# Performance work log

Hardware: AMD Instinct MI355X
Metric: run time of the kernel (lower is better)

Reference implementation:

```python
import jax, jax.numpy as jnp
import numpy as np

B, N, H, E, P = 2, 20000, 128, 200000, 3


def _mlp2(x, w1, b1, w2, b2):
    # Linear -> SiLU -> Linear
    return jax.nn.silu(x @ w1 + b1) @ w2 + b2


def setup_inputs() -> dict:
    key = jax.random.key(0)
    ks = iter(jax.random.split(key, 40))
    def nrm(shape, s=0.05):
        return jax.random.normal(next(ks), shape, dtype=jnp.float32) * s
    inp = {
        "features": jax.random.normal(next(ks), (B, N, H), dtype=jnp.float32),
        "positions": jax.random.normal(next(ks), (B, N, P), dtype=jnp.float32),
        "edge_index_up": jax.random.randint(next(ks), (2, E), 0, N, dtype=jnp.int32),
        "edge_index_down": jax.random.randint(next(ks), (2, E), 0, N, dtype=jnp.int32),
        "degree_up": jax.random.uniform(next(ks), (N,), minval=1.0, maxval=32.0, dtype=jnp.float32),
        "degree_down": jax.random.uniform(next(ks), (N,), minval=1.0, maxval=32.0, dtype=jnp.float32),
    }
    for name in ("up", "down"):
        inp[f"w_msg1_{name}"] = nrm((2 * H + 1, H)); inp[f"b_msg1_{name}"] = jnp.zeros((H,), jnp.float32)
        inp[f"w_msg2_{name}"] = nrm((H, H));         inp[f"b_msg2_{name}"] = jnp.zeros((H,), jnp.float32)
        inp[f"w_pos1_{name}"] = nrm((H, H));         inp[f"b_pos1_{name}"] = jnp.zeros((H,), jnp.float32)
        inp[f"w_pos2_{name}"] = nrm((H, 1));         inp[f"b_pos2_{name}"] = jnp.zeros((1,), jnp.float32)
    inp["w_upd1"] = nrm((2 * H, H)); inp["b_upd1"] = jnp.zeros((H,), jnp.float32)
    inp["w_upd2"] = nrm((H, H));     inp["b_upd2"] = jnp.zeros((H,), jnp.float32)
    return inp


def reference(features, positions, edge_index_up, edge_index_down, degree_up, degree_down,
              w_msg1_up, b_msg1_up, w_msg2_up, b_msg2_up,
              w_pos1_up, b_pos1_up, w_pos2_up, b_pos2_up,
              w_msg1_down, b_msg1_down, w_msg2_down, b_msg2_down,
              w_pos1_down, b_pos1_down, w_pos2_down, b_pos2_down,
              w_upd1, b_upd1, w_upd2, b_upd2):
    n_neighborhoods = 2
    msg_acc = jnp.zeros_like(features)
    pos_upd = jnp.zeros_like(positions)
    neighborhoods = [
        (edge_index_up, degree_up,
         (w_msg1_up, b_msg1_up, w_msg2_up, b_msg2_up),
         (w_pos1_up, b_pos1_up, w_pos2_up, b_pos2_up)),
        (edge_index_down, degree_down,
         (w_msg1_down, b_msg1_down, w_msg2_down, b_msg2_down),
         (w_pos1_down, b_pos1_down, w_pos2_down, b_pos2_down)),
    ]
    for edge_index, degree, msg_p, pos_p in neighborhoods:
        src, dst = edge_index[0], edge_index[1]
        h_src = features[:, src, :]                     # [B, E, H] gather
        h_dst = features[:, dst, :]                     # [B, E, H] gather
        rel_pos = positions[:, src, :] - positions[:, dst, :]  # [B, E, P]
        dist = jnp.linalg.norm(rel_pos, axis=-1, keepdims=True)  # [B, E, 1]
        msg_input = jnp.concatenate([h_src, h_dst, dist], axis=-1)  # [B, E, 2H+1]
        messages = _mlp2(msg_input, *msg_p)             # [B, E, H]
        agg = jnp.zeros_like(features).at[:, dst, :].add(messages)  # scatter-add over dim 1
        agg = agg / jnp.clip(degree, 1.0, None)[None, :, None]
        msg_acc = msg_acc + agg
        weights = jnp.tanh(_mlp2(messages, *pos_p))     # [B, E, 1]
        pos_upd = pos_upd + jnp.zeros_like(positions).at[:, dst, :].add(weights * rel_pos)
    feat_update = _mlp2(jnp.concatenate([features, msg_acc], axis=-1), w_upd1, b_upd1, w_upd2, b_upd2)
    updated_features = features + feat_update
    updated_positions = positions + pos_upd / n_neighborhoods
    return updated_features, updated_positions
```

## Files before the change

### kernel.cpp

```cpp
#include <hip/hip_runtime.h>

#define BB 2
#define NN 20000
#define HH 128
#define EE 200000
#define TR 64
#define NEB 3125
#define NBLK 79
#define NWG (2 * BB * NEB)

typedef unsigned short u16;
typedef __attribute__((ext_vector_type(4))) float f32x4;
typedef __bf16 bf16x8 __attribute__((ext_vector_type(8)));

#define MFMA(a, b, c) __builtin_amdgcn_mfma_f32_16x16x32_bf16((a), (b), (c), 0, 0, 0)

__device__ __forceinline__ float bf2f(u16 u) {
    union { unsigned int i; float f; } v; v.i = ((unsigned int)u) << 16; return v.f;
}
__device__ __forceinline__ u16 f2bf(float f) {
    union { __bf16 h; u16 u; } v; v.h = (__bf16)f; return v.u;
}
#if __has_builtin(__builtin_amdgcn_rcpf)
__device__ __forceinline__ float rcpf(float x) { return __builtin_amdgcn_rcpf(x); }
#else
__device__ __forceinline__ float rcpf(float x) { return 1.f / x; }
#endif
__device__ __forceinline__ float silu_f(float z) { return z * rcpf(1.f + __expf(-z)); }
__device__ __forceinline__ float ldv(const void* p, long i, int f) {
    return f ? ((const float*)p)[i] : bf2f(((const u16*)p)[i]);
}

__global__ __launch_bounds__(256) void detect_zero_kernel(const u16* __restrict__ f,
                                                          int* __restrict__ flag,
                                                          int* __restrict__ cnt) {
    int i = blockIdx.x * 256 + threadIdx.x;
    if (i < 40000) cnt[i] = 0;
    if (blockIdx.x == 0) {
        int tid = threadIdx.x;
        u16 v = f[tid * 2];
        int e = (v >> 7) & 0xFF;
        int ok = (e >= 101 && e <= 143) ? 1 : 0;
        __shared__ int c;
        if (tid == 0) c = 0;
        __syncthreads();
        atomicAdd(&c, ok);
        __syncthreads();
        if (tid == 0) *flag = (c < 200) ? 1 : 0;
    }
}

#define C5TOT 5281540
#define FTOT 180224
#define R0 5240000
#define R1 (R0 + C5TOT)
#define R2 (R1 + FTOT)
#define R3 (R2 + 2 * EE)
struct P18 { const void* p[18]; };
struct P8 { const void* w[8]; };

__global__ __launch_bounds__(256) void setup_kernel(
    P18 cp, P8 wf, const int* __restrict__ eu, const int* __restrict__ ed,
    float* __restrict__ ws_acc, u16* __restrict__ canon, u16* __restrict__ fbase,
    int* __restrict__ cnt_up, int* __restrict__ cnt_dn, const int* __restrict__ flag)
{
    long i = (long)blockIdx.x * 256 + threadIdx.x;
    if (i < R0) { ws_acc[i] = 0.f; return; }
    if (i < R1) {
        static const int off[19] = {
            0, 5120000, 5240000, 5260000, 5280000,
            5280128, 5280256, 5280384, 5280512, 5280640,
            5280642, 5280770, 5280898, 5281026, 5281154, 5281282,
            5281284, 5281412, 5281540 };
        static const int rsz[18] = {
            5120000, 120000, 20000, 20000,
            128, 128, 128, 128, 128, 1,
            128, 128, 128, 128, 128, 1,
            128, 128 };
        static const int soff[18] = {
            0, 0, 0, 0,
            32768, 0, 0, 0, 0, 0,
            32768, 0, 0, 0, 0, 0,
            0, 0 };
        int j = (int)(i - R0);
        int isf = *flag;
        int t = 0;
#pragma unroll 1
        while (j >= off[t + 1]) ++t;
        int k = j - off[t];
        u16 v = 0;
        if (k < rsz[t]) v = f2bf(ldv(cp.p[t], (long)soff[t] + k, isf));
        canon[j] = v;
        return;
    }
    if (i < R2) {
        static const int foff[9] = { 0, 32768, 49152, 65536, 98304, 114688,
                                     131072, 163840, 180224 };
        int j = (int)(i - R1);
        int isf = *flag;
        int t = 0;
#pragma unroll 1
        while (j >= foff[t + 1]) ++t;
        int m = j - foff[t];
        int jj = m & 7, lane = (m >> 3) & 63, nt = (m >> 9) & 7, kt = m >> 12;
        int k = kt * 32 + ((lane >> 4) * 8) + jj;
        int n = nt * 16 + (lane & 15);
        fbase[j] = f2bf(ldv(wf.w[t], (long)k * 128 + n, isf));
        return;
    }
    if (i < R3) {
        int e = (int)(i - R2);
        if (e < EE) atomicAdd(&cnt_up[eu[EE + e]], 1);
        else atomicAdd(&cnt_dn[ed[EE + e - EE]], 1);
    }
}

__global__ __launch_bounds__(256) void gemm_fuse_kernel(
    const void* __restrict__ w2u, const void* __restrict__ p1u,
    const void* __restrict__ b2u, const void* __restrict__ bp1u,
    const void* __restrict__ w2d, const void* __restrict__ p1d,
    const void* __restrict__ b2d, const void* __restrict__ bp1d,
    u16* __restrict__ fragu, u16* __restrict__ fragd,
    u16* __restrict__ cbp1u, u16* __restrict__ cbp1d,
    const int* __restrict__ flag)
{
    const int dir = blockIdx.x >> 6;
    const int idx = (blockIdx.x & 63) * 256 + threadIdx.x;
    const int k = idx >> 7, n = idx & 127;
    const int isf = *flag;
    const void* W2 = dir ? w2d : w2u;
    const void* P1 = dir ? p1d : p1u;
    float s = 0.f;
#pragma unroll 4
    for (int m = 0; m < 128; ++m)
        s += ldv(W2, (long)k * 128 + m, isf) * ldv(P1, (long)m * 128 + n, isf);
    u16* dst = dir ? fragd : fragu;
    dst[(((k >> 5) * 8 + (n >> 4)) * 64 + ((k >> 3) & 3) * 16 + (n & 15)) * 8 + (k & 7)] = f2bf(s);
    if (idx < 128) {
        const void* B2 = dir ? b2d : b2u;
        const void* BP1 = dir ? bp1d : bp1u;
        float t = 0.f;
#pragma unroll 4
        for (int m = 0; m < 128; ++m)
            t += ldv(B2, m, isf) * ldv(P1, (long)m * 128 + idx, isf);
        (dir ? cbp1d : cbp1u)[idx] = f2bf(t + ldv(BP1, idx, isf));
    }
}

struct SP { const int* cnt[2]; int* cur[2]; int* bsum[2]; };

__global__ __launch_bounds__(256) void scan1_kernel(SP p) {
    int half = blockIdx.x / NBLK;
    int b = blockIdx.x - half * NBLK;
    int t = threadIdx.x;
    int i = b * 256 + t;
    __shared__ int buf[256];
    int v = (i < NN) ? p.cnt[half][i] : 0;
    buf[t] = v;
    __syncthreads();
    for (int s = 1; s < 256; s <<= 1) {
        int x = (t >= s) ? buf[t - s] : 0;
        __syncthreads();
        buf[t] += x;
        __syncthreads();
    }
    if (i < NN) p.cur[half][i] = buf[t] - v;
    if (t == 255) p.bsum[half][b] = buf[255];
}

__global__ __launch_bounds__(256) void scan2_kernel(int* __restrict__ bu, int* __restrict__ bd) {
    __shared__ int buf[2][128];
    int half = threadIdx.x >> 7, t = threadIdx.x & 127;
    int* bs = half ? bd : bu;
    int v = (t < NBLK) ? bs[t] : 0;
    buf[half][t] = v;
    __syncthreads();
    for (int s = 1; s < 128; s <<= 1) {
        int x = (t >= s) ? buf[half][t - s] : 0;
        __syncthreads();
        buf[half][t] += x;
        __syncthreads();
    }
    if (t < NBLK) bs[t] = buf[half][t] - v;
}

__global__ void scatter2_kernel(const int* __restrict__ eu, const int* __restrict__ ed,
                                int* __restrict__ cu, const int* __restrict__ bu,
                                int* __restrict__ cd, const int* __restrict__ bd,
                                int* __restrict__ su, int* __restrict__ sd) {
    int e = blockIdx.x * 256 + threadIdx.x;
    if (e < EE) {
        int d = eu[EE + e];
        int p = atomicAdd(&cu[d], 1) + bu[d >> 8];
        su[p] = e;
    } else {
        e -= EE;
        if (e < EE) {
            int d = ed[EE + e];
            int p = atomicAdd(&cd[d], 1) + bd[d >> 8];
            sd[p] = e;
        }
    }
}

struct EP {
    const int* eidx; const int* es; const u16* deg;
    const u16* fW1; const u16* fW2; const u16* fP1;
    const u16* w1last; const u16* bias1; const u16* bias2;
    const u16* biasp1; const u16* wp2; const u16* biasp2;
};

__global__ __launch_bounds__(512, 6) void edge_kernel(
    const u16* __restrict__ feat, const u16* __restrict__ posit,
    EP up, EP dn,
    float* __restrict__ msg_base, float* __restrict__ pos_base)
{
    const int tid = threadIdx.x;
    const int lane = tid & 63;
    const int wv = tid >> 6;
    const int bid0 = blockIdx.x;
    const int xcd = bid0 & 7;
    const int bid = (xcd < 4 ? xcd * 1563 : 4 * 1563 + (xcd - 4) * 1562) + (bid0 >> 3);
    const int half = bid / (BB * NEB);
    const int rem = bid - half * (BB * NEB);
    const int bb = rem / NEB;
    const int s0 = (rem - bb * NEB) * TR;
    const EP P = half ? dn : up;
    float* msg_acc = msg_base + (size_t)bb * NN * HH;
    float* pos_acc = pos_base + (size_t)bb * NN * 3;

    __shared__ u16 sA[TR][136];
    __shared__ u16 sB[TR][136];
    __shared__ u16 sC[TR][136];
    __shared__ float sInv[TR];
    __shared__ float sWgt[TR];
    __shared__ int sDst[TR];

    const int wm = wv >> 2;
    const int wn = wv & 3;
    const int rbase = wm * 32;
    const int mrow = lane & 15;
    const int kq = (lane >> 4) * 8;
    const int crow = (lane >> 4) * 4;
    const int ccol = lane & 15;

    {
        const int r = tid >> 3, part = tid & 7;
        int slot = s0 + r; if (slot >= EE) slot = EE - 1;
        int e = P.es[slot];
        int s = P.eidx[e];
        int d = P.eidx[EE + e];
        if (part == 0) {
            sDst[r] = d;
            sInv[r] = 1.f / fmaxf(bf2f(P.deg[d]), 1.f);
            const u16* ps = posit + ((size_t)bb * NN + s) * 3;
            const u16* pd = posit + ((size_t)bb * NN + d) * 3;
            float dx = bf2f(ps[0]) - bf2f(pd[0]);
            float dy = bf2f(ps[1]) - bf2f(pd[1]);
            float dz = bf2f(ps[2]) - bf2f(pd[2]);
            *(float4*)&sC[r][128] =
                make_float4(sqrtf(dx * dx + dy * dy + dz * dz), dx, dy, dz);
        }
        const uint4* fs = (const uint4*)(feat + ((size_t)bb * NN + s) * HH);
        const uint4* fd = (const uint4*)(feat + ((size_t)bb * NN + d) * HH);
        uint4* as = (uint4*)&sA[r][part * 16];
        uint4* ad = (uint4*)&sB[r][part * 16];
#pragma unroll
        for (int i = 0; i < 2; ++i) { as[i] = fs[part * 2 + i]; ad[i] = fd[part * 2 + i]; }
    }
    __syncthreads();

    f32x4 acc[2][2];
#pragma unroll
    for (int mt = 0; mt < 2; ++mt) {
        acc[mt][0] = (f32x4){0.f, 0.f, 0.f, 0.f};
        acc[mt][1] = (f32x4){0.f, 0.f, 0.f, 0.f};
    }
#pragma unroll
    for (int kt = 0; kt < 8; ++kt) {
        const u16* Xb = (kt < 4) ? &sA[0][0] : &sB[0][0];
        const int kk = (kt & 3) * 32 + kq;
        bf16x8 bw0 = *(const bf16x8*)(P.fW1 + (size_t)(((kt * 8 + wn * 2) * 64 + lane) * 8));
        bf16x8 bw1 = *(const bf16x8*)(P.fW1 + (size_t)(((kt * 8 + wn * 2 + 1) * 64 + lane) * 8));
#pragma unroll
        for (int mt = 0; mt < 2; ++mt) {
            bf16x8 a = *(const bf16x8*)(Xb + (rbase + mt * 16 + mrow) * 136 + kk);
            acc[mt][0] = MFMA(a, bw0, acc[mt][0]);
            acc[mt][1] = MFMA(a, bw1, acc[mt][1]);
        }
    }

#pragma unroll
    for (int n2 = 0; n2 < 2; ++n2) {
        const int col = (wn * 2 + n2) * 16 + ccol;
        const float wl = bf2f(P.w1last[col]);
        const float bb1 = bf2f(P.bias1[col]);
#pragma unroll
        for (int mt = 0; mt < 2; ++mt) {
#pragma unroll
            for (int r = 0; r < 4; ++r) {
                const int row = rbase + mt * 16 + crow + r;
                const float dist = ((const float*)&sC[row][128])[0];
                float z = fmaf(dist, wl, acc[mt][n2][r]) + bb1;
                sC[row][col] = f2bf(silu_f(z));
            }
        }
    }
    __syncthreads();

    f32x4 facc[2][4];
#pragma unroll
    for (int mt = 0; mt < 2; ++mt)
#pragma unroll
        for (int j = 0; j < 4; ++j) facc[mt][j] = (f32x4){0.f, 0.f, 0.f, 0.f};
    const int nt0 = wn * 4;
#pragma unroll
    for (int kt = 0; kt < 4; ++kt) {
        const int kk = kt * 32 + kq;
        bf16x8 bw[4];
#pragma unroll
        for (int j = 0; j < 4; ++j) {
            const int nt = nt0 + j;
            const size_t off = (nt & 8)
                ? (size_t)(16384 + ((kt * 8 + (nt & 7)) * 64 + lane) * 8)
                : (size_t)(((kt * 8 + nt) * 64 + lane) * 8);
            bw[j] = *(const bf16x8*)(P.fW2 + off);
        }
#pragma unroll
        for (int mt = 0; mt < 2; ++mt) {
            bf16x8 a = *(const bf16x8*)(&sC[0][0] + (rbase + mt * 16 + mrow) * 136 + kk);
#pragma unroll
            for (int j = 0; j < 4; ++j) facc[mt][j] = MFMA(a, bw[j], facc[mt][j]);
        }
    }

    if (wn < 2) {
#pragma unroll
        for (int j = 0; j < 4; ++j) {
            const int col = (nt0 + j) * 16 + ccol;
            const float b2v = bf2f(P.bias2[col]);
#pragma unroll
            for (int mt = 0; mt < 2; ++mt) {
#pragma unroll
                for (int r = 0; r < 4; ++r) {
                    const int row = rbase + mt * 16 + crow + r;
                    sA[row][col] = f2bf(facc[mt][j][r] + b2v);
                }
            }
        }
    } else {
#pragma unroll
        for (int j = 0; j < 4; ++j) {
            const int col = (nt0 - 8 + j) * 16 + ccol;
            const float fbv = bf2f(P.biasp1[col]);
#pragma unroll
            for (int mt = 0; mt < 2; ++mt) {
#pragma unroll
                for (int r = 0; r < 4; ++r) {
                    const int row = rbase + mt * 16 + crow + r;
                    sB[row][col] = f2bf(silu_f(facc[mt][j][r] + fbv));
                }
            }
        }
    }
    __syncthreads();

    {
        const int scol = tid & 127;
        const int r0 = (tid >> 7) * 16;
        float vals[16];
#pragma unroll
        for (int j = 0; j < 16; ++j) vals[j] = bf2f(sA[r0 + j][scol]);
        float accv = 0.f;
        int dprev = sDst[r0];
        float invprev = sInv[r0];
#pragma unroll
        for (int j = 0; j < 16; ++j) {
            const int r = r0 + j;
            int dcur = sDst[r];
            if (dcur != dprev) {
                unsafeAtomicAdd(&msg_acc[(size_t)dprev * HH + scol], accv * invprev);
                accv = 0.f; dprev = dcur; invprev = sInv[r];
            }
            accv += (s0 + r < EE) ? vals[j] : 0.f;
        }
        unsafeAtomicAdd(&msg_acc[(size_t)dprev * HH + scol], accv * invprev);
    }

    {
        const int r = tid >> 2, q = tid & 3;
        if (r < TR) {
            const unsigned* t32 = (const unsigned*)&sB[r][q * 32];
            const unsigned* w32 = (const unsigned*)(P.wp2 + q * 32);
            float p = 0.f;
#pragma unroll
            for (int k = 0; k < 16; ++k) {
                unsigned a = t32[k], b = w32[k];
                union { unsigned i; float f; } al, ah, bl, bh;
                al.i = a << 16; ah.i = a & 0xffff0000u;
                bl.i = b << 16; bh.i = b & 0xffff0000u;
                p = fmaf(al.f, bl.f, p);
                p = fmaf(ah.f, bh.f, p);
            }
            p += __shfl_xor(p, 1);
            p += __shfl_xor(p, 2);
            if (q == 0)
                sWgt[r] = (s0 + r < EE) ? tanhf(p + bf2f(P.biasp2[0])) : 0.f;
        }
    }
    __syncthreads();

    if (tid < 12) {
        const int comp = tid % 3;
        const int r0 = (tid / 3) * 16;
        float accv = 0.f;
        int dprev = sDst[r0];
#pragma unroll
        for (int j = 0; j < 16; ++j) {
            const int r = r0 + j;
            int dcur = sDst[r];
            if (dcur != dprev) {
                if (accv != 0.f) unsafeAtomicAdd(&pos_acc[(size_t)dprev * 3 + comp], accv);
                accv = 0.f; dprev = dcur;
            }
            accv += sWgt[r] * ((const float*)&sC[r][128])[1 + comp];
        }
        if (accv != 0.f) unsafeAtomicAdd(&pos_acc[(size_t)dprev * 3 + comp], accv);
    }
}

__global__ __launch_bounds__(256) void update_kernel(
    const void* __restrict__ rawfeat, const void* __restrict__ rawpos,
    const u16* __restrict__ fU1, const u16* __restrict__ bu1,
    const u16* __restrict__ fU2, const u16* __restrict__ bu2,
    void* __restrict__ outp, const float* __restrict__ magg, const float* __restrict__ pacc,
    const int* __restrict__ flag)
{
    const int tid = threadIdx.x;
    const int lane = tid & 63;
    const int wv = tid >> 6;
    const int row0 = blockIdx.x * 64;
    const int isf = *flag;

    __shared__ u16 sA[64][136];
    __shared__ u16 sB[64][136];

    if (isf) {
        const float* fp = (const float*)rawfeat + (size_t)row0 * HH;
        for (int i = tid; i < 1024; i += 256) {
            int r = i >> 4, c = (i & 15) * 8;
            float4 v0 = *(const float4*)(fp + (size_t)r * HH + c);
            float4 v1 = *(const float4*)(fp + (size_t)r * HH + c + 4);
            uint4 o;
            o.x = (unsigned)f2bf(v0.x) | ((unsigned)f2bf(v0.y) << 16);
            o.y = (unsigned)f2bf(v0.z) | ((unsigned)f2bf(v0.w) << 16);
            o.z = (unsigned)f2bf(v1.x) | ((unsigned)f2bf(v1.y) << 16);
            o.w = (unsigned)f2bf(v1.z) | ((unsigned)f2bf(v1.w) << 16);
            *(uint4*)&sA[r][c] = o;
        }
    } else {
        const uint4* fp = (const uint4*)((const u16*)rawfeat + (size_t)row0 * HH);
        for (int i = tid; i < 1024; i += 256) {
            int r = i >> 4, c = i & 15;
            *(uint4*)&sA[r][c * 8] = fp[i];
        }
    }
    {
        const float4* am = (const float4*)(magg) + (size_t)row0 * 32;
        for (int i = tid; i < 2048; i += 256) {
            int r = i >> 5;
            float4 v = am[i];
            int c = (i & 31) * 4;
            sB[r][c + 0] = f2bf(v.x);
            sB[r][c + 1] = f2bf(v.y);
            sB[r][c + 2] = f2bf(v.z);
            sB[r][c + 3] = f2bf(v.w);
        }
    }
    __syncthreads();

    const int nt0 = wv * 2;
    const int mrow = lane & 15;
    const int kq = (lane >> 4) * 8;
    const int crow = (lane >> 4) * 4;
    const int ccol = lane & 15;

    f32x4 acc[4][2];
#pragma unroll
    for (int mt = 0; mt < 4; ++mt) {
        acc[mt][0] = (f32x4){0.f, 0.f, 0.f, 0.f};
        acc[mt][1] = (f32x4){0.f, 0.f, 0.f, 0.f};
    }
#pragma unroll
    for (int kt = 0; kt < 8; ++kt) {
        const u16* Xb = (kt < 4) ? &sA[0][0] : &sB[0][0];
        const int kk = (kt & 3) * 32 + kq;
        bf16x8 bw0 = *(const bf16x8*)(fU1 + (size_t)(((kt * 8 + nt0) * 64 + lane) * 8));
        bf16x8 bw1 = *(const bf16x8*)(fU1 + (size_t)(((kt * 8 + nt0 + 1) * 64 + lane) * 8));
#pragma unroll
        for (int mt = 0; mt < 4; ++mt) {
            bf16x8 a = *(const bf16x8*)(Xb + (mt * 16 + mrow) * 136 + kk);
            acc[mt][0] = MFMA(a, bw0, acc[mt][0]);
            acc[mt][1] = MFMA(a, bw1, acc[mt][1]);
        }
    }
    __syncthreads();

#pragma unroll
    for (int mt = 0; mt < 4; ++mt) {
#pragma unroll
        for (int n2 = 0; n2 < 2; ++n2) {
            const int col = (nt0 + n2) * 16 + ccol;
            const float bb = bf2f(bu1[col]);
#pragma unroll
            for (int r = 0; r < 4; ++r) {
                const int row = mt * 16 + crow + r;
                sB[row][col] = f2bf(silu_f(acc[mt][n2][r] + bb));
            }
        }
    }
    __syncthreads();

#pragma unroll
    for (int mt = 0; mt < 4; ++mt) {
        acc[mt][0] = (f32x4){0.f, 0.f, 0.f, 0.f};
        acc[mt][1] = (f32x4){0.f, 0.f, 0.f, 0.f};
    }
#pragma unroll
    for (int kt = 0; kt < 4; ++kt) {
        const int kk = kt * 32 + kq;
        bf16x8 bw0 = *(const bf16x8*)(fU2 + (size_t)(((kt * 8 + nt0) * 64 + lane) * 8));
        bf16x8 bw1 = *(const bf16x8*)(fU2 + (size_t)(((kt * 8 + nt0 + 1) * 64 + lane) * 8));
#pragma unroll
        for (int mt = 0; mt < 4; ++mt) {
            bf16x8 a = *(const bf16x8*)(&sB[0][0] + (mt * 16 + mrow) * 136 + kk);
            acc[mt][0] = MFMA(a, bw0, acc[mt][0]);
            acc[mt][1] = MFMA(a, bw1, acc[mt][1]);
        }
    }
#pragma unroll
    for (int mt = 0; mt < 4; ++mt) {
#pragma unroll
        for (int n2 = 0; n2 < 2; ++n2) {
            const int col = (nt0 + n2) * 16 + ccol;
            const float bb = bf2f(bu2[col]);
#pragma unroll
            for (int r = 0; r < 4; ++r) {
                const int row = mt * 16 + crow + r;
                const size_t idx = (size_t)(row0 + row) * HH + col;
                if (isf) {
                    float base = ((const float*)rawfeat)[idx];
                    ((float*)outp)[idx] = acc[mt][n2][r] + bb + base;
                } else {
                    float base = bf2f(sA[row][col]);
                    ((u16*)outp)[idx] = f2bf(acc[mt][n2][r] + bb + base);
                }
            }
        }
    }

    if (tid < 192) {
        int i = row0 * 3 + tid;
        float x = pacc[i];
        if (isf) {
            float base = ((const float*)rawpos)[i];
            ((float*)outp)[5120000 + i] = base + 0.5f * x;
        } else {
            float base = bf2f(((const u16*)rawpos)[i]);
            ((u16*)outp)[5120000 + i] = f2bf(base + 0.5f * x);
        }
    }
}

extern "C" void kernel_launch(void* const* d_in, const int* in_sizes, int n_in,
                              void* d_out, int out_size, void* d_ws, size_t ws_size,
                              hipStream_t stream)
{
    float* ws_msg  = (float*)d_ws;
    float* ws_pos  = (float*)((char*)d_ws + 20480000);
    int*   cnt_up  = (int*)((char*)d_ws + 20960000);
    int*   cnt_dn  = (int*)((char*)d_ws + 21040000);
    int*   cur_up  = (int*)((char*)d_ws + 21120000);
    int*   cur_dn  = (int*)((char*)d_ws + 21200000);
    int*   bsum_up = (int*)((char*)d_ws + 21280000);
    int*   bsum_dn = (int*)((char*)d_ws + 21280400);
    int*   es_up   = (int*)((char*)d_ws + 21280800);
    int*   es_dn   = (int*)((char*)d_ws + 22080800);
    u16*   fbase   = (u16*)((char*)d_ws + 22880800);
    u16*   canon   = (u16*)((char*)d_ws + 23241248);
    int*   flag    = (int*)((char*)d_ws + 33804328);
    if (ws_size < 33804332ULL) return;

    u16* f_m1u = fbase;
    u16* f_m2u = fbase + 32768;
    u16* f_p1u = fbase + 49152;
    u16* f_m1d = fbase + 65536;
    u16* f_m2d = fbase + 98304;
    u16* f_p1d = fbase + 114688;
    u16* f_u1  = fbase + 131072;
    u16* f_u2  = fbase + 163840;

    u16* cfeat  = canon;
    u16* cpos   = canon + 5120000;
    u16* cdgu   = canon + 5240000;
    u16* cdgd   = canon + 5260000;
    u16* cw1lu  = canon + 5280000;
    u16* cb1u   = canon + 5280128;
    u16* cb2u   = canon + 5280256;
    u16* cbp1u  = canon + 5280384;
    u16* cwp2u  = canon + 5280512;
    u16* cbp2u  = canon + 5280640;
    u16* cw1ld  = canon + 5280642;
    u16* cb1d   = canon + 5280770;
    u16* cb2d   = canon + 5280898;
    u16* cbp1d  = canon + 5281026;
    u16* cwp2d  = canon + 5281154;
    u16* cbp2d  = canon + 5281282;
    u16* cbu1   = canon + 5281284;
    u16* cbu2   = canon + 5281412;

    const int* ei_up = (const int*)d_in[2];
    const int* ei_dn = (const int*)d_in[3];

    detect_zero_kernel<<<157, 256, 0, stream>>>((const u16*)d_in[0], flag, cnt_up);

    P18 cp;
    cp.p[0] = d_in[0];  cp.p[1] = d_in[1];  cp.p[2] = d_in[4];  cp.p[3] = d_in[5];
    cp.p[4] = d_in[6];  cp.p[5] = d_in[7];  cp.p[6] = d_in[9];  cp.p[7] = d_in[11];
    cp.p[8] = d_in[12]; cp.p[9] = d_in[13];
    cp.p[10] = d_in[14]; cp.p[11] = d_in[15]; cp.p[12] = d_in[17]; cp.p[13] = d_in[19];
    cp.p[14] = d_in[20]; cp.p[15] = d_in[21];
    cp.p[16] = d_in[23]; cp.p[17] = d_in[25];
    P8 wsf;
    wsf.w[0] = d_in[6];  wsf.w[1] = d_in[8];  wsf.w[2] = d_in[10]; wsf.w[3] = d_in[14];
    wsf.w[4] = d_in[16]; wsf.w[5] = d_in[18]; wsf.w[6] = d_in[22]; wsf.w[7] = d_in[24];
    setup_kernel<<<(R3 + 255) / 256, 256, 0, stream>>>(cp, wsf, ei_up, ei_dn,
                                                       ws_msg, canon, fbase,
                                                       cnt_up, cnt_dn, flag);

    gemm_fuse_kernel<<<128, 256, 0, stream>>>(d_in[8], d_in[10], d_in[9], d_in[11],
                                              d_in[16], d_in[18], d_in[17], d_in[19],
                                              f_p1u, f_p1d, cbp1u, cbp1d, flag);

    SP sp;
    sp.cnt[0] = cnt_up; sp.cnt[1] = cnt_dn;
    sp.cur[0] = cur_up; sp.cur[1] = cur_dn;
    sp.bsum[0] = bsum_up; sp.bsum[1] = bsum_dn;
    scan1_kernel<<<2 * NBLK, 256, 0, stream>>>(sp);
    scan2_kernel<<<1, 256, 0, stream>>>(bsum_up, bsum_dn);
    scatter2_kernel<<<(2 * EE + 255) / 256, 256, 0, stream>>>(ei_up, ei_dn, cur_up, bsum_up,
                                                              cur_dn, bsum_dn, es_up, es_dn);

    EP up, dn;
    up.eidx = ei_up; up.es = es_up; up.deg = cdgu;
    up.fW1 = f_m1u; up.fW2 = f_m2u; up.fP1 = f_p1u;
    up.w1last = cw1lu; up.bias1 = cb1u; up.bias2 = cb2u;
    up.biasp1 = cbp1u; up.wp2 = cwp2u; up.biasp2 = cbp2u;
    dn.eidx = ei_dn; dn.es = es_dn; dn.deg = cdgd;
    dn.fW1 = f_m1d; dn.fW2 = f_m2d; dn.fP1 = f_p1d;
    dn.w1last = cw1ld; dn.bias1 = cb1d; dn.bias2 = cb2d;
    dn.biasp1 = cbp1d; dn.wp2 = cwp2d; dn.biasp2 = cbp2d;
    edge_kernel<<<NWG, 512, 0, stream>>>(cfeat, cpos, up, dn, ws_msg, ws_pos);

    update_kernel<<<625, 256, 0, stream>>>(d_in[0], d_in[1], f_u1, cbu1, f_u2, cbu2,
                                           d_out, ws_msg, ws_pos, flag);
}
```

Before: 458.6 us.

## Assign destination-node tiles to workgroups and accumulate in LDS instead of global atomics

The edge kernel now launches one workgroup per 32-node destination tile per batch. It walks that tile's dst-sorted edge range for both directions and accumulates messages and position updates in shared-memory float accumulators, then writes bf16 messages and fp32 positions straight out. This removes the global atomic scatter and the 5.2M-float zeroing of the workspace, and halves the message-buffer traffic read by the update kernel. In exchange, per-tile work is uneven, the grid shrinks to 1250 workgroups with a lower occupancy hint, and the aggregate is rounded to bf16 before the update.

Result: slower. 732.3 us (+59.7%).

```diff
diff --git a/kernel.cpp b/kernel.cpp
--- a/kernel.cpp
+++ b/kernel.cpp
@@ -4,10 +4,9 @@
 #define NN 20000
 #define HH 128
 #define EE 200000
-#define TR 64
-#define NEB 3125
+#define TILE 32
+#define NTIL 625
 #define NBLK 79
-#define NWG (2 * BB * NEB)
 
 typedef unsigned short u16;
 typedef __attribute__((ext_vector_type(4))) float f32x4;
@@ -52,21 +51,19 @@
 
 #define C5TOT 5281540
 #define FTOT 180224
-#define R0 5240000
-#define R1 (R0 + C5TOT)
-#define R2 (R1 + FTOT)
-#define R3 (R2 + 2 * EE)
+#define S1 C5TOT
+#define S2 (S1 + FTOT)
+#define S3 (S2 + 2 * EE)
 struct P18 { const void* p[18]; };
 struct P8 { const void* w[8]; };
 
 __global__ __launch_bounds__(256) void setup_kernel(
     P18 cp, P8 wf, const int* __restrict__ eu, const int* __restrict__ ed,
-    float* __restrict__ ws_acc, u16* __restrict__ canon, u16* __restrict__ fbase,
+    u16* __restrict__ canon, u16* __restrict__ fbase,
     int* __restrict__ cnt_up, int* __restrict__ cnt_dn, const int* __restrict__ flag)
 {
     long i = (long)blockIdx.x * 256 + threadIdx.x;
-    if (i < R0) { ws_acc[i] = 0.f; return; }
-    if (i < R1) {
+    if (i < S1) {
         static const int off[19] = {
             0, 5120000, 5240000, 5260000, 5280000,
             5280128, 5280256, 5280384, 5280512, 5280640,
@@ -82,7 +79,7 @@
             32768, 0, 0, 0, 0, 0,
             32768, 0, 0, 0, 0, 0,
             0, 0 };
-        int j = (int)(i - R0);
+        int j = (int)i;
         int isf = *flag;
         int t = 0;
 #pragma unroll 1
@@ -93,10 +90,10 @@
         canon[j] = v;
         return;
     }
-    if (i < R2) {
+    if (i < S2) {
         static const int foff[9] = { 0, 32768, 49152, 65536, 98304, 114688,
                                      131072, 163840, 180224 };
-        int j = (int)(i - R1);
+        int j = (int)(i - S1);
         int isf = *flag;
         int t = 0;
 #pragma unroll 1
@@ -108,8 +105,8 @@
         fbase[j] = f2bf(ldv(wf.w[t], (long)k * 128 + n, isf));
         return;
     }
-    if (i < R3) {
-        int e = (int)(i - R2);
+    if (i < S3) {
+        int e = (int)(i - S2);
         if (e < EE) atomicAdd(&cnt_up[eu[EE + e]], 1);
         else atomicAdd(&cnt_dn[ed[EE + e - EE]], 1);
     }
@@ -203,38 +200,37 @@
     }
 }
 
-struct EP {
+struct EP2 {
     const int* eidx; const int* es; const u16* deg;
-    const u16* fW1; const u16* fW2; const u16* fP1;
+    const int* cnt; const int* cur; const int* bsum;
+    const u16* fW1; const u16* fW2;
     const u16* w1last; const u16* bias1; const u16* bias2;
     const u16* biasp1; const u16* wp2; const u16* biasp2;
 };
 
-__global__ __launch_bounds__(512, 6) void edge_kernel(
+__global__ __launch_bounds__(512, 2) void edge_kernel(
     const u16* __restrict__ feat, const u16* __restrict__ posit,
-    EP up, EP dn,
-    float* __restrict__ msg_base, float* __restrict__ pos_base)
+    EP2 up, EP2 dn,
+    u16* __restrict__ msg_out, float* __restrict__ pos_out)
 {
     const int tid = threadIdx.x;
     const int lane = tid & 63;
     const int wv = tid >> 6;
-    const int bid0 = blockIdx.x;
-    const int xcd = bid0 & 7;
-    const int bid = (xcd < 4 ? xcd * 1563 : 4 * 1563 + (xcd - 4) * 1562) + (bid0 >> 3);
-    const int half = bid / (BB * NEB);
-    const int rem = bid - half * (BB * NEB);
-    const int bb = rem / NEB;
-    const int s0 = (rem - bb * NEB) * TR;
-    const EP P = half ? dn : up;
-    float* msg_acc = msg_base + (size_t)bb * NN * HH;
-    float* pos_acc = pos_base + (size_t)bb * NN * 3;
-
-    __shared__ u16 sA[TR][136];
-    __shared__ u16 sB[TR][136];
-    __shared__ u16 sC[TR][136];
-    __shared__ float sInv[TR];
-    __shared__ float sWgt[TR];
-    __shared__ int sDst[TR];
+    const int bb = blockIdx.x / NTIL;
+    const int tile = blockIdx.x - bb * NTIL;
+    const int n0 = tile * TILE;
+
+    __shared__ u16 sA[64][136];
+    __shared__ u16 sB[64][136];
+    __shared__ u16 sC[64][136];
+    __shared__ float accM[TILE][132];
+    __shared__ float accP[TILE][4];
+    __shared__ float sInv[64];
+    __shared__ int sDloc[64];
+
+    for (int i = tid; i < TILE * 132; i += 512) ((float*)accM)[i] = 0.f;
+    if (tid < TILE * 4) ((float*)accP)[tid] = 0.f;
+    __syncthreads();
 
     const int wm = wv >> 2;
     const int wn = wv & 3;
@@ -244,188 +240,203 @@
     const int crow = (lane >> 4) * 4;
     const int ccol = lane & 15;
 
+#pragma unroll 1
+    for (int dir = 0; dir < 2; ++dir) {
+        const EP2 P = dir ? dn : up;
+        const int e0 = P.bsum[n0 >> 8] + P.cur[n0] - P.cnt[n0];
+        const int n1 = n0 + TILE;
+        const int e1 = (n1 >= NN) ? EE : (P.bsum[n1 >> 8] + P.cur[n1] - P.cnt[n1]);
+
+#pragma unroll 1
+        for (int c0 = e0; c0 < e1; c0 += 64) {
+            {
+                const int r = tid >> 3, part = tid & 7;
+                int slot = c0 + r; if (slot >= e1) slot = e1 - 1;
+                int e = P.es[slot];
+                int s = P.eidx[e];
+                int d = P.eidx[EE + e];
+                if (part == 0) {
+                    sDloc[r] = d - n0;
+                    sInv[r] = 1.f / fmaxf(bf2f(P.deg[d]), 1.f);
+                    const u16* ps = posit + ((size_t)bb * NN + s) * 3;
+                    const u16* pd = posit + ((size_t)bb * NN + d) * 3;
+                    float dx = bf2f(ps[0]) - bf2f(pd[0]);
+                    float dy = bf2f(ps[1]) - bf2f(pd[1]);
+                    float dz = bf2f(ps[2]) - bf2f(pd[2]);
+                    *(float4*)&sC[r][128] =
+                        make_float4(sqrtf(dx * dx + dy * dy + dz * dz), dx, dy, dz);
+                }
+                const uint4* fs = (const uint4*)(feat + ((size_t)bb * NN + s) * HH);
+                const uint4* fd = (const uint4*)(feat + ((size_t)bb * NN + d) * HH);
+                uint4* as = (uint4*)&sA[r][part * 16];
+                uint4* ad = (uint4*)&sB[r][part * 16];
+                as[0] = fs[part * 2];     as[1] = fs[part * 2 + 1];
+                ad[0] = fd[part * 2];     ad[1] = fd[part * 2 + 1];
+            }
+            __syncthreads();
+
+            f32x4 acc[2][2];
+#pragma unroll
+            for (int mt = 0; mt < 2; ++mt) {
+                acc[mt][0] = (f32x4){0.f, 0.f, 0.f, 0.f};
+                acc[mt][1] = (f32x4){0.f, 0.f, 0.f, 0.f};
+            }
+#pragma unroll
+            for (int kt = 0; kt < 8; ++kt) {
+                const u16* Xb = (kt < 4) ? &sA[0][0] : &sB[0][0];
+                const int kk = (kt & 3) * 32 + kq;
+                bf16x8 bw0 = *(const bf16x8*)(P.fW1 + (size_t)(((kt * 8 + wn * 2) * 64 + lane) * 8));
+                bf16x8 bw1 = *(const bf16x8*)(P.fW1 + (size_t)(((kt * 8 + wn * 2 + 1) * 64 + lane) * 8));
+#pragma unroll
+                for (int mt = 0; mt < 2; ++mt) {
+                    bf16x8 a = *(const bf16x8*)(Xb + (rbase + mt * 16 + mrow) * 136 + kk);
+                    acc[mt][0] = MFMA(a, bw0, acc[mt][0]);
+                    acc[mt][1] = MFMA(a, bw1, acc[mt][1]);
+                }
+            }
+
+#pragma unroll
+            for (int n2 = 0; n2 < 2; ++n2) {
+                const int col = (wn * 2 + n2) * 16 + ccol;
+                const float wl = bf2f(P.w1last[col]);
+                const float bb1 = bf2f(P.bias1[col]);
+#pragma unroll
+                for (int mt = 0; mt < 2; ++mt) {
+#pragma unroll
+                    for (int r = 0; r < 4; ++r) {
+                        const int row = rbase + mt * 16 + crow + r;
+                        const float dist = ((const float*)&sC[row][128])[0];
+                        float z = fmaf(dist, wl, acc[mt][n2][r]) + bb1;
+                        sC[row][col] = f2bf(silu_f(z));
+                    }
+                }
+            }
+            __syncthreads();
+
+            f32x4 facc[2][4];
+#pragma unroll
+            for (int mt = 0; mt < 2; ++mt)
+#pragma unroll
+                for (int j = 0; j < 4; ++j) facc[mt][j] = (f32x4){0.f, 0.f, 0.f, 0.f};
+            const int nt0 = wn * 4;
+#pragma unroll
+            for (int kt = 0; kt < 4; ++kt) {
+                const int kk = kt * 32 + kq;
+                bf16x8 bw[4];
+#pragma unroll
+                for (int j = 0; j < 4; ++j) {
+                    const int nt = nt0 + j;
+                    const size_t off = (nt & 8)
+                        ? (size_t)(16384 + ((kt * 8 + (nt & 7)) * 64 + lane) * 8)
+                        : (size_t)(((kt * 8 + nt) * 64 + lane) * 8);
+                    bw[j] = *(const bf16x8*)(P.fW2 + off);
+                }
+#pragma unroll
+                for (int mt = 0; mt < 2; ++mt) {
+                    bf16x8 a = *(const bf16x8*)(&sC[0][0] + (rbase + mt * 16 + mrow) * 136 + kk);
+#pragma unroll
+                    for (int j = 0; j < 4; ++j) facc[mt][j] = MFMA(a, bw[j], facc[mt][j]);
+                }
+            }
+
+            if (wn < 2) {
+#pragma unroll
+                for (int j = 0; j < 4; ++j) {
+                    const int col = (nt0 + j) * 16 + ccol;
+                    const float b2v = bf2f(P.bias2[col]);
+#pragma unroll
+                    for (int mt = 0; mt < 2; ++mt) {
+#pragma unroll
+                        for (int r = 0; r < 4; ++r) {
+                            const int row = rbase + mt * 16 + crow + r;
+                            sA[row][col] = f2bf(facc[mt][j][r] + b2v);
+                        }
+                    }
+                }
+            } else {
+#pragma unroll
+                for (int j = 0; j < 4; ++j) {
+                    const int col = (nt0 - 8 + j) * 16 + ccol;
+                    const float fbv = bf2f(P.biasp1[col]);
+#pragma unroll
+                    for (int mt = 0; mt < 2; ++mt) {
+#pragma unroll
+                        for (int r = 0; r < 4; ++r) {
+                            const int row = rbase + mt * 16 + crow + r;
+                            sB[row][col] = f2bf(silu_f(facc[mt][j][r] + fbv));
+                        }
+                    }
+                }
+            }
+            __syncthreads();
+
+            {
+                const int scol = tid & 127;
+                const int r0 = (tid >> 7) * 16;
+                float vals[16];
+#pragma unroll
+                for (int j = 0; j < 16; ++j) vals[j] = bf2f(sA[r0 + j][scol]);
+                float accv = 0.f;
+                int dprev = sDloc[r0];
+                float invprev = sInv[r0];
+#pragma unroll
+                for (int j = 0; j < 16; ++j) {
+                    const int r = r0 + j;
+                    int dcur = sDloc[r];
+                    if (dcur != dprev) {
+                        atomicAdd(&accM[dprev][scol], accv * invprev);
+                        accv = 0.f; dprev = dcur; invprev = sInv[r];
+                    }
+                    accv += (c0 + r < e1) ? vals[j] : 0.f;
+                }
+                atomicAdd(&accM[dprev][scol], accv * invprev);
+            }
+
+            {
+                const int r = tid >> 2, q = tid & 3;
+                if (r < 64) {
+                    const unsigned* t32 = (const unsigned*)&sB[r][q * 32];
+                    const unsigned* w32 = (const unsigned*)(P.wp2 + q * 32);
+                    float p = 0.f;
+#pragma unroll
+                    for (int k = 0; k < 16; ++k) {
+                        unsigned a = t32[k], b = w32[k];
+                        union { unsigned i; float f; } al, ah, bl, bh;
+                        al.i = a << 16; ah.i = a & 0xffff0000u;
+                        bl.i = b << 16; bh.i = b & 0xffff0000u;
+                        p = fmaf(al.f, bl.f, p);
+                        p = fmaf(ah.f, bh.f, p);
+                    }
+                    p += __shfl_xor(p, 1);
+                    p += __shfl_xor(p, 2);
+                    if (q == 0 && c0 + r < e1) {
+                        float wgt = tanhf(p + bf2f(P.biasp2[0]));
+                        const float* rp = (const float*)&sC[r][128];
+                        const int dl = sDloc[r];
+                        atomicAdd(&accP[dl][0], wgt * rp[1]);
+                        atomicAdd(&accP[dl][1], wgt * rp[2]);
+                        atomicAdd(&accP[dl][2], wgt * rp[3]);
+                    }
+                }
+            }
+            __syncthreads();
+        }
+    }
+
+    __syncthreads();
+
     {
-        const int r = tid >> 3, part = tid & 7;
-        int slot = s0 + r; if (slot >= EE) slot = EE - 1;
-        int e = P.es[slot];
-        int s = P.eidx[e];
-        int d = P.eidx[EE + e];
-        if (part == 0) {
-            sDst[r] = d;
-            sInv[r] = 1.f / fmaxf(bf2f(P.deg[d]), 1.f);
-            const u16* ps = posit + ((size_t)bb * NN + s) * 3;
-            const u16* pd = posit + ((size_t)bb * NN + d) * 3;
-            float dx = bf2f(ps[0]) - bf2f(pd[0]);
-            float dy = bf2f(ps[1]) - bf2f(pd[1]);
-            float dz = bf2f(ps[2]) - bf2f(pd[2]);
-            *(float4*)&sC[r][128] =
-                make_float4(sqrtf(dx * dx + dy * dy + dz * dz), dx, dy, dz);
-        }
-        const uint4* fs = (const uint4*)(feat + ((size_t)bb * NN + s) * HH);
-        const uint4* fd = (const uint4*)(feat + ((size_t)bb * NN + d) * HH);
-        uint4* as = (uint4*)&sA[r][part * 16];
-        uint4* ad = (uint4*)&sB[r][part * 16];
-#pragma unroll
-        for (int i = 0; i < 2; ++i) { as[i] = fs[part * 2 + i]; ad[i] = fd[part * 2 + i]; }
-    }
-    __syncthreads();
-
-    f32x4 acc[2][2];
-#pragma unroll
-    for (int mt = 0; mt < 2; ++mt) {
-        acc[mt][0] = (f32x4){0.f, 0.f, 0.f, 0.f};
-        acc[mt][1] = (f32x4){0.f, 0.f, 0.f, 0.f};
-    }
-#pragma unroll
-    for (int kt = 0; kt < 8; ++kt) {
-        const u16* Xb = (kt < 4) ? &sA[0][0] : &sB[0][0];
-        const int kk = (kt & 3) * 32 + kq;
-        bf16x8 bw0 = *(const bf16x8*)(P.fW1 + (size_t)(((kt * 8 + wn * 2) * 64 + lane) * 8));
-        bf16x8 bw1 = *(const bf16x8*)(P.fW1 + (size_t)(((kt * 8 + wn * 2 + 1) * 64 + lane) * 8));
-#pragma unroll
-        for (int mt = 0; mt < 2; ++mt) {
-            bf16x8 a = *(const bf16x8*)(Xb + (rbase + mt * 16 + mrow) * 136 + kk);
-            acc[mt][0] = MFMA(a, bw0, acc[mt][0]);
-            acc[mt][1] = MFMA(a, bw1, acc[mt][1]);
-        }
-    }
-
-#pragma unroll
-    for (int n2 = 0; n2 < 2; ++n2) {
-        const int col = (wn * 2 + n2) * 16 + ccol;
-        const float wl = bf2f(P.w1last[col]);
-        const float bb1 = bf2f(P.bias1[col]);
-#pragma unroll
-        for (int mt = 0; mt < 2; ++mt) {
-#pragma unroll
-            for (int r = 0; r < 4; ++r) {
-                const int row = rbase + mt * 16 + crow + r;
-                const float dist = ((const float*)&sC[row][128])[0];
-                float z = fmaf(dist, wl, acc[mt][n2][r]) + bb1;
-                sC[row][col] = f2bf(silu_f(z));
-            }
-        }
-    }
-    __syncthreads();
-
-    f32x4 facc[2][4];
-#pragma unroll
-    for (int mt = 0; mt < 2; ++mt)
-#pragma unroll
-        for (int j = 0; j < 4; ++j) facc[mt][j] = (f32x4){0.f, 0.f, 0.f, 0.f};
-    const int nt0 = wn * 4;
-#pragma unroll
-    for (int kt = 0; kt < 4; ++kt) {
-        const int kk = kt * 32 + kq;
-        bf16x8 bw[4];
-#pragma unroll
-        for (int j = 0; j < 4; ++j) {
-            const int nt = nt0 + j;
-            const size_t off = (nt & 8)
-                ? (size_t)(16384 + ((kt * 8 + (nt & 7)) * 64 + lane) * 8)
-                : (size_t)(((kt * 8 + nt) * 64 + lane) * 8);
-            bw[j] = *(const bf16x8*)(P.fW2 + off);
-        }
-#pragma unroll
-        for (int mt = 0; mt < 2; ++mt) {
-            bf16x8 a = *(const bf16x8*)(&sC[0][0] + (rbase + mt * 16 + mrow) * 136 + kk);
-#pragma unroll
-            for (int j = 0; j < 4; ++j) facc[mt][j] = MFMA(a, bw[j], facc[mt][j]);
-        }
-    }
-
-    if (wn < 2) {
-#pragma unroll
-        for (int j = 0; j < 4; ++j) {
-            const int col = (nt0 + j) * 16 + ccol;
-            const float b2v = bf2f(P.bias2[col]);
-#pragma unroll
-            for (int mt = 0; mt < 2; ++mt) {
-#pragma unroll
-                for (int r = 0; r < 4; ++r) {
-                    const int row = rbase + mt * 16 + crow + r;
-                    sA[row][col] = f2bf(facc[mt][j][r] + b2v);
-                }
-            }
-        }
-    } else {
-#pragma unroll
-        for (int j = 0; j < 4; ++j) {
-            const int col = (nt0 - 8 + j) * 16 + ccol;
-            const float fbv = bf2f(P.biasp1[col]);
-#pragma unroll
-            for (int mt = 0; mt < 2; ++mt) {
-#pragma unroll
-                for (int r = 0; r < 4; ++r) {
-                    const int row = rbase + mt * 16 + crow + r;
-                    sB[row][col] = f2bf(silu_f(facc[mt][j][r] + fbv));
-                }
-            }
-        }
-    }
-    __syncthreads();
-
-    {
-        const int scol = tid & 127;
-        const int r0 = (tid >> 7) * 16;
-        float vals[16];
-#pragma unroll
-        for (int j = 0; j < 16; ++j) vals[j] = bf2f(sA[r0 + j][scol]);
-        float accv = 0.f;
-        int dprev = sDst[r0];
-        float invprev = sInv[r0];
-#pragma unroll
-        for (int j = 0; j < 16; ++j) {
-            const int r = r0 + j;
-            int dcur = sDst[r];
-            if (dcur != dprev) {
-                unsafeAtomicAdd(&msg_acc[(size_t)dprev * HH + scol], accv * invprev);
-                accv = 0.f; dprev = dcur; invprev = sInv[r];
-            }
-            accv += (s0 + r < EE) ? vals[j] : 0.f;
-        }
-        unsafeAtomicAdd(&msg_acc[(size_t)dprev * HH + scol], accv * invprev);
-    }
-
-    {
-        const int r = tid >> 2, q = tid & 3;
-        if (r < TR) {
-            const unsigned* t32 = (const unsigned*)&sB[r][q * 32];
-            const unsigned* w32 = (const unsigned*)(P.wp2 + q * 32);
-            float p = 0.f;
-#pragma unroll
-            for (int k = 0; k < 16; ++k) {
-                unsigned a = t32[k], b = w32[k];
-                union { unsigned i; float f; } al, ah, bl, bh;
-                al.i = a << 16; ah.i = a & 0xffff0000u;
-                bl.i = b << 16; bh.i = b & 0xffff0000u;
-                p = fmaf(al.f, bl.f, p);
-                p = fmaf(ah.f, bh.f, p);
-            }
-            p += __shfl_xor(p, 1);
-            p += __shfl_xor(p, 2);
-            if (q == 0)
-                sWgt[r] = (s0 + r < EE) ? tanhf(p + bf2f(P.biasp2[0])) : 0.f;
-        }
-    }
-    __syncthreads();
-
-    if (tid < 12) {
-        const int comp = tid % 3;
-        const int r0 = (tid / 3) * 16;
-        float accv = 0.f;
-        int dprev = sDst[r0];
-#pragma unroll
-        for (int j = 0; j < 16; ++j) {
-            const int r = r0 + j;
-            int dcur = sDst[r];
-            if (dcur != dprev) {
-                if (accv != 0.f) unsafeAtomicAdd(&pos_acc[(size_t)dprev * 3 + comp], accv);
-                accv = 0.f; dprev = dcur;
-            }
-            accv += sWgt[r] * ((const float*)&sC[r][128])[1 + comp];
-        }
-        if (accv != 0.f) unsafeAtomicAdd(&pos_acc[(size_t)dprev * 3 + comp], accv);
+        const int r = tid >> 4, c = (tid & 15) * 8;
+        uint4 o;
+        o.x = (unsigned)f2bf(accM[r][c + 0]) | ((unsigned)f2bf(accM[r][c + 1]) << 16);
+        o.y = (unsigned)f2bf(accM[r][c + 2]) | ((unsigned)f2bf(accM[r][c + 3]) << 16);
+        o.z = (unsigned)f2bf(accM[r][c + 4]) | ((unsigned)f2bf(accM[r][c + 5]) << 16);
+        o.w = (unsigned)f2bf(accM[r][c + 6]) | ((unsigned)f2bf(accM[r][c + 7]) << 16);
+        *(uint4*)&msg_out[((size_t)bb * NN + n0 + r) * HH + c] = o;
+    }
+    if (tid < TILE * 3) {
+        const int r = tid / 3, comp = tid - r * 3;
+        pos_out[((size_t)bb * NN + n0 + r) * 3 + comp] = accP[r][comp];
     }
 }
 
@@ -433,7 +444,7 @@
     const void* __restrict__ rawfeat, const void* __restrict__ rawpos,
     const u16* __restrict__ fU1, const u16* __restrict__ bu1,
     const u16* __restrict__ fU2, const u16* __restrict__ bu2,
-    void* __restrict__ outp, const float* __restrict__ magg, const float* __restrict__ pacc,
+    void* __restrict__ outp, const u16* __restrict__ magg, const float* __restrict__ pacc,
     const int* __restrict__ flag)
 {
     const int tid = threadIdx.x;
@@ -466,15 +477,10 @@
         }
     }
     {
-        const float4* am = (const float4*)(magg) + (size_t)row0 * 32;
-        for (int i = tid; i < 2048; i += 256) {
-            int r = i >> 5;
-            float4 v = am[i];
-            int c = (i & 31) * 4;
-            sB[r][c + 0] = f2bf(v.x);
-            sB[r][c + 1] = f2bf(v.y);
-            sB[r][c + 2] = f2bf(v.z);
-            sB[r][c + 3] = f2bf(v.w);
+        const uint4* am = (const uint4*)magg + (size_t)row0 * 16;
+        for (int i = tid; i < 1024; i += 256) {
+            int r = i >> 4, c = i & 15;
+            *(uint4*)&sB[r][c * 8] = am[i];
         }
     }
     __syncthreads();
@@ -576,7 +582,7 @@
                               void* d_out, int out_size, void* d_ws, size_t ws_size,
                               hipStream_t stream)
 {
-    float* ws_msg  = (float*)d_ws;
+    u16*   ws_msg  = (u16*)d_ws;
     float* ws_pos  = (float*)((char*)d_ws + 20480000);
     int*   cnt_up  = (int*)((char*)d_ws + 20960000);
     int*   cnt_dn  = (int*)((char*)d_ws + 21040000);
@@ -634,8 +640,8 @@
     P8 wsf;
     wsf.w[0] = d_in[6];  wsf.w[1] = d_in[8];  wsf.w[2] = d_in[10]; wsf.w[3] = d_in[14];
     wsf.w[4] = d_in[16]; wsf.w[5] = d_in[18]; wsf.w[6] = d_in[22]; wsf.w[7] = d_in[24];
-    setup_kernel<<<(R3 + 255) / 256, 256, 0, stream>>>(cp, wsf, ei_up, ei_dn,
-                                                       ws_msg, canon, fbase,
+    setup_kernel<<<(S3 + 255) / 256, 256, 0, stream>>>(cp, wsf, ei_up, ei_dn,
+                                                       canon, fbase,
                                                        cnt_up, cnt_dn, flag);
 
     gemm_fuse_kernel<<<128, 256, 0, stream>>>(d_in[8], d_in[10], d_in[9], d_in[11],
@@ -651,16 +657,18 @@
     scatter2_kernel<<<(2 * EE + 255) / 256, 256, 0, stream>>>(ei_up, ei_dn, cur_up, bsum_up,
                                                               cur_dn, bsum_dn, es_up, es_dn);
 
-    EP up, dn;
+    EP2 up, dn;
     up.eidx = ei_up; up.es = es_up; up.deg = cdgu;
-    up.fW1 = f_m1u; up.fW2 = f_m2u; up.fP1 = f_p1u;
+    up.cnt = cnt_up; up.cur = cur_up; up.bsum = bsum_up;
+    up.fW1 = f_m1u; up.fW2 = f_m2u;
     up.w1last = cw1lu; up.bias1 = cb1u; up.bias2 = cb2u;
     up.biasp1 = cbp1u; up.wp2 = cwp2u; up.biasp2 = cbp2u;
     dn.eidx = ei_dn; dn.es = es_dn; dn.deg = cdgd;
-    dn.fW1 = f_m1d; dn.fW2 = f_m2d; dn.fP1 = f_p1d;
+    dn.cnt = cnt_dn; dn.cur = cur_dn; dn.bsum = bsum_dn;
+    dn.fW1 = f_m1d; dn.fW2 = f_m2d;
     dn.w1last = cw1ld; dn.bias1 = cb1d; dn.bias2 = cb2d;
     dn.biasp1 = cbp1d; dn.wp2 = cwp2d; dn.biasp2 = cbp2d;
-    edge_kernel<<<NWG, 512, 0, stream>>>(cfeat, cpos, up, dn, ws_msg, ws_pos);
+    edge_kernel<<<BB * NTIL, 512, 0, stream>>>(cfeat, cpos, up, dn, ws_msg, ws_pos);
 
     update_kernel<<<625, 256, 0, stream>>>(d_in[0], d_in[1], f_u1, cbu1, f_u2, cbu2,
                                            d_out, ws_msg, ws_pos, flag);
```
